# Performance work log

Measured on AMD Instinct MI355X. Metric: run time of the kernel, lower is better.

## Reference

```python
import jax, jax.numpy as jnp
import numpy as np

IN_CH = 32
OUT_CH = 32
M1, M2 = 32, 32
BS, H, W = 8, 256, 256


def setup_inputs() -> dict:
    key = jax.random.key(0)
    kx, kk = jax.random.split(key)
    x = jax.random.normal(kx, (BS, IN_CH, H, W), dtype=jnp.float32)
    # reset_parameters: randn * (1/(in_ch*out_ch)) + 1
    scale = 1.0 / (IN_CH * OUT_CH)
    kernel = jax.random.normal(kk, (2, 1, OUT_CH, M1, M2, 2), dtype=jnp.float32) * scale + 1.0
    r = jnp.float32(1.0)
    return {"x": x, "kernel": kernel, "r": r}


def reference(x, kernel, r):
    # view_as_complex: last dim of 2 -> complex, shape [2, 1, C, M1, M2]
    kc = (kernel[..., 0] + 1j * kernel[..., 1]).astype(jnp.complex64)
    # elementwise complex power kernel**r
    kc = jnp.power(kc, r)

    # forward 2D real FFT over spatial dims (ortho norm)
    x_ft = jnp.fft.rfftn(x, axes=(-2, -1), norm="ortho")  # [bs, C, H, W//2+1]
    Hf, Wr = x_ft.shape[-2], x_ft.shape[-1]
    n1 = min(Hf // 2, M1)
    n2 = min(Wr, M2)

    def mix(block, k):
        # fft over channel dim (-3), multiply by complex kernel, ifft back
        b = jnp.fft.fft(block, axis=-3, norm="ortho")
        b = b * k[..., :n1, :n2]
        return jnp.fft.ifft(b, axis=-3, norm="ortho")

    pos = mix(x_ft[..., :n1, :n2], kc[0])          # low positive freqs
    neg = mix(x_ft[..., Hf - n1:, :n2], kc[1])     # low negative freqs

    out_ft = jnp.zeros((x.shape[0], OUT_CH, Hf, Wr), dtype=jnp.complex64)
    out_ft = out_ft.at[..., :n1, :n2].set(pos)
    out_ft = out_ft.at[..., Hf - n1:, :n2].set(neg)

    # inverse real FFT back to spatial domain
    return jnp.fft.irfftn(out_ft, s=(x.shape[-2], x.shape[-1]), axes=(-2, -1), norm="ortho")
```

## Files before the change

### kernel.cpp

```cpp
#include <hip/hip_runtime.h>
#include <math.h>


#define TWO_PI 6.28318530717958647692f

typedef _Float16 half8 __attribute__((ext_vector_type(8)));
typedef float float4v __attribute__((ext_vector_type(4)));

__global__ __launch_bounds__(256) void kPX(const float* __restrict__ kin,
                                           const float* __restrict__ rp,
                                           float2* __restrict__ kp,
                                           _Float16* __restrict__ Bf) {
  const int tid = threadIdx.x;
  if (blockIdx.x < 256) {
    const int i = blockIdx.x * 256 + tid;
    const float r = rp[0];
    const float kr = kin[2 * i], ki = kin[2 * i + 1];
    const float m2 = fmaf(kr, kr, ki * ki);
    float2 o = make_float2(0.f, 0.f);
    if (m2 > 0.f) {
      const float lm = 0.5f * logf(m2);
      const float ang = atan2f(ki, kr);
      const float mag = expf(r * lm);
      float s, c;
      sincosf(r * ang, &s, &c);
      o = make_float2(mag * c, mag * s);
    }
    kp[i] = o;
  } else {
    const int f0 = ((blockIdx.x - 256) * 256 + tid) * 2;
#pragma unroll
    for (int u = 0; u < 2; ++u) {
      const int f = f0 + u;
      const int i = f & 7;
      const int lane = (f >> 3) & 63;
      const int kk = (f >> 9) & 1;
      const int n = f >> 10;
      const int k = kk * 32 + ((lane >> 4) << 3) + i;
      const int w = k >> 1, cs = k & 1;
      const int xc = n * 16 + (lane & 15);
      const float sc = (w ? 2.0f : 1.0f) / 256.0f;
      float s, c;
      sincosf(TWO_PI * (float)((w * xc) & 255) / 256.0f, &s, &c);
      Bf[f] = (_Float16)(cs ? (-s * sc) : (c * sc));
    }
  }
}

__global__ __launch_bounds__(256) void kA(const float* __restrict__ x,
                                          float2* __restrict__ z1) {
  __shared__ float xs[8192];
  const int tid = threadIdx.x;
  const long row0 = (long)blockIdx.x * 32;
  const float* xg = x + row0 * 256;
  {
    const int xl = tid & 31, rq = tid >> 5;
    const float* xgr = xg + rq * 4 * 256 + xl;
#pragma unroll
    for (int cb = 0; cb < 8; ++cb) {
      const int xc = xl + 32 * cb;
      const float4 v = make_float4(xgr[32 * cb], xgr[32 * cb + 256],
                                   xgr[32 * cb + 512], xgr[32 * cb + 768]);
      *(float4*)(xs + xc * 32 + 4 * ((rq + xc) & 7)) = v;
    }
  }
  __syncthreads();
  const float RT = 0.70710678118654752440f;
#pragma unroll
  for (int k = 0; k < 4; ++k) {
    const int i = tid + (k << 8);
    const int x1 = i >> 5, r = i & 31;
    float* base = xs + x1 * 32 + ((r + 4 * x1) & 31);
    const float a0 = base[0],        a1 = base[1024],     a2 = base[2048];
    const float a3 = base[3 * 1024], a4 = base[4 * 1024], a5 = base[5 * 1024];
    const float a6 = base[6 * 1024], a7 = base[7 * 1024];
    const float t0 = a0 + a4, t1 = a0 - a4, t2 = a2 + a6, t3 = a2 - a6;
    const float u0 = a1 + a5, u1 = a1 - a5, u2 = a3 + a7, u3 = a3 - a7;
    const float E0 = t0 + t2, O0 = u0 + u2;
    const float d1 = RT * (u1 - u3), d2 = RT * (u1 + u3);
    base[0]        = E0 + O0;
    base[1024]     = E0 - O0;
    base[2 * 1024] = t1 + d1;
    base[3 * 1024] = -(t3 + d2);
    base[4 * 1024] = t0 - t2;
    base[5 * 1024] = -(u0 - u2);
    base[6 * 1024] = t1 - d1;
    base[7 * 1024] = t3 - d2;
  }
  __syncthreads();
  const int w = tid & 31;
  const int r0 = (tid >> 5) << 2;
  const int p = w & 7;
  int pr, pi;
  float si;
  if (p == 0)      { pr = 0;           pi = 0;      si = 0.f; }
  else if (p == 4) { pr = 1;           pi = 1;      si = 0.f; }
  else if (p < 4)  { pr = 2 * p;       pi = pr + 1; si = 1.f; }
  else             { pr = 2 * (8 - p); pi = pr + 1; si = -1.f; }
  const char* ur = (const char*)xs + pr * 4096;
  const char* ui = (const char*)xs + pi * 4096;
  const char* urp[8];
  const char* uip[8];
#pragma unroll
  for (int j = 0; j < 8; ++j) {
    const int off = 4 * ((r0 + 4 * j) & 31) + 128 * j;
    urp[j] = ur + off;
    uip[j] = ui + off;
  }
  float s1, c1;
  sincosf(-TWO_PI * (float)w / 256.0f, &s1, &c1);
  float pc = 1.f, ps = 0.f;
  float Cr0 = 0, Cr1 = 0, Cr2 = 0, Cr3 = 0;
  float Ci0 = 0, Ci1 = 0, Ci2 = 0, Ci3 = 0;
#pragma unroll
  for (int bq = 0; bq < 4; ++bq) {
#pragma unroll
    for (int j = 0; j < 8; ++j) {
      const float4 Fr = *(const float4*)(urp[j] + bq * 1024);
      const float4 Fi = *(const float4*)(uip[j] + bq * 1024);
      const float qs = si * ps, qc = si * pc;
      Cr0 = fmaf(Fr.x, pc, fmaf(-Fi.x, qs, Cr0));
      Ci0 = fmaf(Fr.x, ps, fmaf( Fi.x, qc, Ci0));
      Cr1 = fmaf(Fr.y, pc, fmaf(-Fi.y, qs, Cr1));
      Ci1 = fmaf(Fr.y, ps, fmaf( Fi.y, qc, Ci1));
      Cr2 = fmaf(Fr.z, pc, fmaf(-Fi.z, qs, Cr2));
      Ci2 = fmaf(Fr.z, ps, fmaf( Fi.z, qc, Ci2));
      Cr3 = fmaf(Fr.w, pc, fmaf(-Fi.w, qs, Cr3));
      Ci3 = fmaf(Fr.w, ps, fmaf( Fi.w, qc, Ci3));
      const float tn = fmaf(pc, c1, -ps * s1);
      ps = fmaf(pc, s1, ps * c1);
      pc = tn;
    }
  }
  float2* o = z1 + (row0 + r0) * 32 + w;
  o[0]  = make_float2(Cr0, Ci0);
  o[32] = make_float2(Cr1, Ci1);
  o[64] = make_float2(Cr2, Ci2);
  o[96] = make_float2(Cr3, Ci3);
}

__global__ __launch_bounds__(256) void kB(const float2* __restrict__ z1,
                                          float2* __restrict__ z2) {
  __shared__ float2 zs[8192];
  const int tid = threadIdx.x;
  const int bc = blockIdx.x >> 1, th = blockIdx.x & 1;
  {
    const float4* s4 = (const float4*)(z1 + (long)bc * 8192);
    float4* d4 = (float4*)zs;
    for (int i = tid; i < 4096; i += 256) d4[i] = s4[i];
  }
  __syncthreads();
  const float RT = 0.70710678118654752440f;
#pragma unroll
  for (int e = 0; e < 4; ++e) {
    float2* base = zs + tid + (e << 8);
    float2 a[8];
#pragma unroll
    for (int j = 0; j < 8; ++j) a[j] = base[j * 1024];
    float2 t0 = make_float2(a[0].x + a[4].x, a[0].y + a[4].y);
    float2 t1 = make_float2(a[0].x - a[4].x, a[0].y - a[4].y);
    float2 t2 = make_float2(a[2].x + a[6].x, a[2].y + a[6].y);
    float2 t3 = make_float2(a[2].x - a[6].x, a[2].y - a[6].y);
    const float2 E0 = make_float2(t0.x + t2.x, t0.y + t2.y);
    const float2 E2 = make_float2(t0.x - t2.x, t0.y - t2.y);
    const float2 E1 = make_float2(t1.x + t3.y, t1.y - t3.x);
    const float2 E3 = make_float2(t1.x - t3.y, t1.y + t3.x);
    t0 = make_float2(a[1].x + a[5].x, a[1].y + a[5].y);
    t1 = make_float2(a[1].x - a[5].x, a[1].y - a[5].y);
    t2 = make_float2(a[3].x + a[7].x, a[3].y + a[7].y);
    t3 = make_float2(a[3].x - a[7].x, a[3].y - a[7].y);
    const float2 O0 = make_float2(t0.x + t2.x, t0.y + t2.y);
    const float2 O2 = make_float2(t0.x - t2.x, t0.y - t2.y);
    const float2 O1 = make_float2(t1.x + t3.y, t1.y - t3.x);
    const float2 O3 = make_float2(t1.x - t3.y, t1.y + t3.x);
    const float2 B0 = O0;
    const float2 B1 = make_float2(RT * (O1.x + O1.y), RT * (O1.y - O1.x));
    const float2 B2 = make_float2(O2.y, -O2.x);
    const float2 B3 = make_float2(RT * (O3.y - O3.x), -RT * (O3.x + O3.y));
    base[0]        = make_float2(E0.x + B0.x, E0.y + B0.y);
    base[1 * 1024] = make_float2(E1.x + B1.x, E1.y + B1.y);
    base[2 * 1024] = make_float2(E2.x + B2.x, E2.y + B2.y);
    base[3 * 1024] = make_float2(E3.x + B3.x, E3.y + B3.y);
    base[4 * 1024] = make_float2(E0.x - B0.x, E0.y - B0.y);
    base[5 * 1024] = make_float2(E1.x - B1.x, E1.y - B1.y);
    base[6 * 1024] = make_float2(E2.x - B2.x, E2.y - B2.y);
    base[7 * 1024] = make_float2(E3.x - B3.x, E3.y - B3.y);
  }
  __syncthreads();
  const int w = tid & 31;
  const int lt = tid >> 5;
  const int t0i = th * 32 + lt;
  const int hbase = th ? (192 + t0i) : t0i;
  float stc[4], sts[4], pcq[4], psq[4], ar[4], ai[4];
#pragma unroll
  for (int q = 0; q < 4; ++q) {
    sincosf(-TWO_PI * (float)(hbase + 8 * q) / 256.0f, &sts[q], &stc[q]);
    pcq[q] = 1.f; psq[q] = 0.f; ar[q] = 0.f; ai[q] = 0.f;
  }
  const float2* sp = zs + lt * 1024 + w;
  for (int y1 = 0; y1 < 32; ++y1) {
    const float2 v = sp[y1 * 32];
#pragma unroll
    for (int q = 0; q < 4; ++q) {
      ar[q] = fmaf(v.x, pcq[q], fmaf(-v.y, psq[q], ar[q]));
      ai[q] = fmaf(v.x, psq[q], fmaf( v.y, pcq[q], ai[q]));
      const float tn = fmaf(pcq[q], stc[q], -psq[q] * sts[q]);
      psq[q] = fmaf(pcq[q], sts[q], psq[q] * stc[q]);
      pcq[q] = tn;
    }
  }
  float2* dst = z2 + (long)bc * 2048 + t0i * 32 + w;
#pragma unroll
  for (int q = 0; q < 4; ++q) dst[q * 256] = make_float2(ar[q], ai[q]);
}

__global__ __launch_bounds__(256) void kC(const float2* __restrict__ z2,
                                          const float2* __restrict__ kp,
                                          float2* __restrict__ g) {
  __shared__ float2 z2s[8 * 33];
  __shared__ float2 fk[8 * 33];
  __shared__ float2 tw[32];
  const int tid = threadIdx.x;
  if (tid < 32) {
    float s, c;
    sincosf(-TWO_PI * (float)tid / 32.0f, &s, &c);
    tw[tid] = make_float2(c, s);
  }
  const int m0 = blockIdx.x * 8;
  const int b = m0 >> 11;
  const int twi = m0 & 2047;
  const int t = twi >> 5;
  const int w0 = twi & 31;
  const int s_ = t >> 5, tm = t & 31;
  {
    const int ci = tid >> 3, wj = tid & 7;
    z2s[wj * 33 + ci] = z2[((long)(b * 32 + ci)) * 2048 + t * 32 + w0 + wj];
  }
  __syncthreads();
  const int m = tid & 7;
  {
    const int cf = tid >> 3;
    float fr = 0, fi = 0;
    int i0 = 0;
#pragma unroll 8
    for (int ci = 0; ci < 32; ++ci) {
      const float2 z = z2s[m * 33 + ci];
      const float2 t0 = tw[i0]; i0 = (i0 + cf) & 31;
      fr = fmaf(z.x, t0.x, fmaf(-z.y, t0.y, fr));
      fi = fmaf(z.x, t0.y, fmaf( z.y, t0.x, fi));
    }
    const float2 k0 = kp[((s_ * 32 + cf) * 32 + tm) * 32 + w0 + m];
    fk[m * 33 + cf] = make_float2(fr * k0.x - fi * k0.y, fr * k0.y + fi * k0.x);
  }
  __syncthreads();
  {
    const int co = tid >> 3;
    float gr = 0, gi = 0;
    int i0 = 0;
#pragma unroll 8
    for (int cf = 0; cf < 32; ++cf) {
      const float2 f = fk[m * 33 + cf];
      const float2 t0 = tw[i0]; i0 = (i0 + co) & 31;
      gr = fmaf(f.x, t0.x, fmaf( f.y, t0.y, gr));
      gi = fmaf(f.y, t0.x, fmaf(-f.x, t0.y, gi));
    }
    const float SC = 1.0f / 8192.0f;
    g[((long)(b * 32 + co)) * 2048 + t * 32 + w0 + m] = make_float2(gr * SC, gi * SC);
  }
}

__global__ __launch_bounds__(512) void kDE2(const float2* __restrict__ g,
                                            const _Float16* __restrict__ Bf,
                                            float* __restrict__ out) {
  __shared__ float smem[32 * 260];
  __shared__ _Float16 tst2[32 * 68];
  float2* gs = (float2*)smem;
  float* ot = smem;
  const int tid = threadIdx.x;
  const int bc = blockIdx.x >> 1, yh = blockIdx.x & 1;
  const int lane = tid & 63, l15 = lane & 15, lg = lane >> 4;
  uint4 bfr[2][2];
#pragma unroll
  for (int nn = 0; nn < 2; ++nn)
#pragma unroll
    for (int kk = 0; kk < 2; ++kk) {
      const int n = 2 * (tid >> 6) + nn;
      bfr[nn][kk] = *(const uint4*)(Bf + (((n * 2 + kk) * 64) + lane) * 8);
    }
  {
    const float4* s4 = (const float4*)(g + (long)bc * 2048);
    float4* d4 = (float4*)gs;
    for (int i = tid; i < 1024; i += 512) d4[i] = s4[i];
  }
  __syncthreads();
  const int w = tid & 31;
  float Ur[2][8], Ui[2][8];
#pragma unroll
  for (int e = 0; e < 2; ++e) {
    const int y1 = (tid + (e << 9)) >> 5;
#pragma unroll
    for (int p = 0; p < 8; ++p) { Ur[e][p] = 0.f; Ui[e][p] = 0.f; }
    float s1, c1;
    sincosf(TWO_PI * (float)y1 / 256.0f, &s1, &c1);
    float pc = 1.f, ps = 0.f;
#pragma unroll
    for (int t = 0; t < 64; ++t) {
      if (t == 32) {
        float s2, c2;
        sincosf(TWO_PI * (float)((224 * y1) & 255) / 256.0f, &s2, &c2);
        pc = c2; ps = s2;
      }
      const float2 v = gs[t * 32 + w];
      const int k = t & 7;
      Ur[e][k] = fmaf(v.x, pc, fmaf(-v.y, ps, Ur[e][k]));
      Ui[e][k] = fmaf(v.x, ps, fmaf( v.y, pc, Ui[e][k]));
      const float tn = fmaf(pc, c1, -ps * s1);
      ps = fmaf(pc, s1, ps * c1);
      pc = tn;
    }
  }
  const long rb0 = (long)bc * 256;
#pragma unroll
  for (int yql = 0; yql < 4; ++yql) {
    const int yq = yh * 4 + yql;
    {
      float sqv, cqv;
      sincosf(TWO_PI * (float)yq / 8.0f, &sqv, &cqv);
#pragma unroll
      for (int e = 0; e < 2; ++e) {
        const int y1 = (tid + (e << 9)) >> 5;
        float tr = 0.f, ti = 0.f, qc = 1.f, qs = 0.f;
#pragma unroll
        for (int p = 0; p < 8; ++p) {
          tr = fmaf(Ur[e][p], qc, fmaf(-Ui[e][p], qs, tr));
          ti = fmaf(Ur[e][p], qs, fmaf( Ui[e][p], qc, ti));
          const float tn = fmaf(qc, cqv, -qs * sqv);
          qs = fmaf(qc, sqv, qs * cqv);
          qc = tn;
        }
        union { unsigned int u; _Float16 h[2]; } hu;
        hu.h[0] = (_Float16)tr;
        hu.h[1] = (_Float16)ti;
        *(unsigned int*)&tst2[y1 * 68 + 2 * w] = hu.u;
      }
    }
    __syncthreads();
    {
      half8 afr[2][2];
#pragma unroll
      for (int rt = 0; rt < 2; ++rt)
#pragma unroll
        for (int kk = 0; kk < 2; ++kk) {
          const _Float16* ap = tst2 + (rt * 16 + l15) * 68 + kk * 32 + lg * 8;
          const uint2 lo = *(const uint2*)ap;
          const uint2 hi = *(const uint2*)(ap + 4);
          uint4 u4;
          u4.x = lo.x; u4.y = lo.y; u4.z = hi.x; u4.w = hi.y;
          afr[rt][kk] = __builtin_bit_cast(half8, u4);
        }
#pragma unroll
      for (int rt = 0; rt < 2; ++rt)
#pragma unroll
        for (int nn = 0; nn < 2; ++nn) {
          float4v acc = {0.f, 0.f, 0.f, 0.f};
          acc = __builtin_amdgcn_mfma_f32_16x16x32_f16(
              afr[rt][0], __builtin_bit_cast(half8, bfr[nn][0]), acc, 0, 0, 0);
          acc = __builtin_amdgcn_mfma_f32_16x16x32_f16(
              afr[rt][1], __builtin_bit_cast(half8, bfr[nn][1]), acc, 0, 0, 0);
          const int n = 2 * (tid >> 6) + nn;
          const int col = n * 16 + l15;
          const int r0l = rt * 16 + lg * 4;
          ot[(r0l + 0) * 260 + col] = acc[0];
          ot[(r0l + 1) * 260 + col] = acc[1];
          ot[(r0l + 2) * 260 + col] = acc[2];
          ot[(r0l + 3) * 260 + col] = acc[3];
        }
    }
    __syncthreads();
    {
      const long rbase = rb0 + yq * 32;
#pragma unroll
      for (int rd = 0; rd < 4; ++rd) {
        const int f = tid + (rd << 9);
        const int row = f >> 6;
        const int c4 = f & 63;
        const float4 v = *(const float4*)(ot + row * 260 + c4 * 4);
        *(float4*)(out + (rbase + row) * 256 + c4 * 4) = v;
      }
    }
  }
}

extern "C" void kernel_launch(void* const* d_in, const int* in_sizes, int n_in,
                              void* d_out, int out_size, void* d_ws, size_t ws_size,
                              hipStream_t stream) {
  const float* x = (const float*)d_in[0];
  const float* kin = (const float*)d_in[1];
  const float* rp = (const float*)d_in[2];
  float* out = (float*)d_out;
  char* ws = (char*)d_ws;

  float2* z1 = (float2*)(ws);
  float2* z2 = (float2*)(ws + (16ull << 20));
  float2* kp = (float2*)(ws + (24ull << 20));
  _Float16* Bf = (_Float16*)(ws + (25ull << 20));
  float2* g  = (float2*)(ws);

  kPX<<<288, 256, 0, stream>>>(kin, rp, kp, Bf);
  kA<<<2048, 256, 0, stream>>>(x, z1);
  kB<<<512, 256, 0, stream>>>(z1, z2);
  kC<<<2048, 256, 0, stream>>>(z2, kp, g);
  kDE2<<<512, 512, 0, stream>>>(g, Bf, out);
}
```

Before: 182.8 us.

## Replace row-wise partial DFT in kA with fp16 MFMA matmul against twiddle table

```diff
diff --git a/kernel.cpp b/kernel.cpp
--- a/kernel.cpp
+++ b/kernel.cpp
@@ -10,7 +10,8 @@
 __global__ __launch_bounds__(256) void kPX(const float* __restrict__ kin,
                                            const float* __restrict__ rp,
                                            float2* __restrict__ kp,
-                                           _Float16* __restrict__ Bf) {
+                                           _Float16* __restrict__ Bf,
+                                           _Float16* __restrict__ Ef) {
   const int tid = threadIdx.x;
   if (blockIdx.x < 256) {
     const int i = blockIdx.x * 256 + tid;
@@ -27,7 +28,7 @@
       o = make_float2(mag * c, mag * s);
     }
     kp[i] = o;
-  } else {
+  } else if (blockIdx.x < 288) {
     const int f0 = ((blockIdx.x - 256) * 256 + tid) * 2;
 #pragma unroll
     for (int u = 0; u < 2; ++u) {
@@ -44,99 +45,69 @@
       sincosf(TWO_PI * (float)((w * xc) & 255) / 256.0f, &s, &c);
       Bf[f] = (_Float16)(cs ? (-s * sc) : (c * sc));
     }
-  }
-}
-
-__global__ __launch_bounds__(256) void kA(const float* __restrict__ x,
-                                          float2* __restrict__ z1) {
-  __shared__ float xs[8192];
+  } else {
+    const int f0 = ((blockIdx.x - 288) * 256 + tid) * 2;
+#pragma unroll
+    for (int u = 0; u < 2; ++u) {
+      const int f = f0 + u;
+      const int i = f & 7;
+      const int lane = (f >> 3) & 63;
+      const int seg = f >> 9;
+      const int kk = seg & 7, nn = seg >> 3;
+      const int k = kk * 32 + ((lane >> 4) << 3) + i;
+      const int n = nn * 16 + (lane & 15);
+      const int w = n >> 1, cs = n & 1;
+      float s, c;
+      sincosf(TWO_PI * (float)((w * k) & 255) / 256.0f, &s, &c);
+      Ef[f] = (_Float16)(cs ? -s : c);
+    }
+  }
+}
+
+__global__ __launch_bounds__(256) void kA3(const float* __restrict__ x,
+                                           const _Float16* __restrict__ Ef,
+                                           float* __restrict__ z1f) {
+  __shared__ _Float16 As[8192];
   const int tid = threadIdx.x;
   const long row0 = (long)blockIdx.x * 32;
-  const float* xg = x + row0 * 256;
-  {
-    const int xl = tid & 31, rq = tid >> 5;
-    const float* xgr = xg + rq * 4 * 256 + xl;
-#pragma unroll
-    for (int cb = 0; cb < 8; ++cb) {
-      const int xc = xl + 32 * cb;
-      const float4 v = make_float4(xgr[32 * cb], xgr[32 * cb + 256],
-                                   xgr[32 * cb + 512], xgr[32 * cb + 768]);
-      *(float4*)(xs + xc * 32 + 4 * ((rq + xc) & 7)) = v;
-    }
-  }
-  __syncthreads();
-  const float RT = 0.70710678118654752440f;
-#pragma unroll
-  for (int k = 0; k < 4; ++k) {
-    const int i = tid + (k << 8);
-    const int x1 = i >> 5, r = i & 31;
-    float* base = xs + x1 * 32 + ((r + 4 * x1) & 31);
-    const float a0 = base[0],        a1 = base[1024],     a2 = base[2048];
-    const float a3 = base[3 * 1024], a4 = base[4 * 1024], a5 = base[5 * 1024];
-    const float a6 = base[6 * 1024], a7 = base[7 * 1024];
-    const float t0 = a0 + a4, t1 = a0 - a4, t2 = a2 + a6, t3 = a2 - a6;
-    const float u0 = a1 + a5, u1 = a1 - a5, u2 = a3 + a7, u3 = a3 - a7;
-    const float E0 = t0 + t2, O0 = u0 + u2;
-    const float d1 = RT * (u1 - u3), d2 = RT * (u1 + u3);
-    base[0]        = E0 + O0;
-    base[1024]     = E0 - O0;
-    base[2 * 1024] = t1 + d1;
-    base[3 * 1024] = -(t3 + d2);
-    base[4 * 1024] = t0 - t2;
-    base[5 * 1024] = -(u0 - u2);
-    base[6 * 1024] = t1 - d1;
-    base[7 * 1024] = t3 - d2;
-  }
-  __syncthreads();
-  const int w = tid & 31;
-  const int r0 = (tid >> 5) << 2;
-  const int p = w & 7;
-  int pr, pi;
-  float si;
-  if (p == 0)      { pr = 0;           pi = 0;      si = 0.f; }
-  else if (p == 4) { pr = 1;           pi = 1;      si = 0.f; }
-  else if (p < 4)  { pr = 2 * p;       pi = pr + 1; si = 1.f; }
-  else             { pr = 2 * (8 - p); pi = pr + 1; si = -1.f; }
-  const char* ur = (const char*)xs + pr * 4096;
-  const char* ui = (const char*)xs + pi * 4096;
-  const char* urp[8];
-  const char* uip[8];
-#pragma unroll
-  for (int j = 0; j < 8; ++j) {
-    const int off = 4 * ((r0 + 4 * j) & 31) + 128 * j;
-    urp[j] = ur + off;
-    uip[j] = ui + off;
-  }
-  float s1, c1;
-  sincosf(-TWO_PI * (float)w / 256.0f, &s1, &c1);
-  float pc = 1.f, ps = 0.f;
-  float Cr0 = 0, Cr1 = 0, Cr2 = 0, Cr3 = 0;
-  float Ci0 = 0, Ci1 = 0, Ci2 = 0, Ci3 = 0;
-#pragma unroll
-  for (int bq = 0; bq < 4; ++bq) {
-#pragma unroll
-    for (int j = 0; j < 8; ++j) {
-      const float4 Fr = *(const float4*)(urp[j] + bq * 1024);
-      const float4 Fi = *(const float4*)(uip[j] + bq * 1024);
-      const float qs = si * ps, qc = si * pc;
-      Cr0 = fmaf(Fr.x, pc, fmaf(-Fi.x, qs, Cr0));
-      Ci0 = fmaf(Fr.x, ps, fmaf( Fi.x, qc, Ci0));
-      Cr1 = fmaf(Fr.y, pc, fmaf(-Fi.y, qs, Cr1));
-      Ci1 = fmaf(Fr.y, ps, fmaf( Fi.y, qc, Ci1));
-      Cr2 = fmaf(Fr.z, pc, fmaf(-Fi.z, qs, Cr2));
-      Ci2 = fmaf(Fr.z, ps, fmaf( Fi.z, qc, Ci2));
-      Cr3 = fmaf(Fr.w, pc, fmaf(-Fi.w, qs, Cr3));
-      Ci3 = fmaf(Fr.w, ps, fmaf( Fi.w, qc, Ci3));
-      const float tn = fmaf(pc, c1, -ps * s1);
-      ps = fmaf(pc, s1, ps * c1);
-      pc = tn;
-    }
-  }
-  float2* o = z1 + (row0 + r0) * 32 + w;
-  o[0]  = make_float2(Cr0, Ci0);
-  o[32] = make_float2(Cr1, Ci1);
-  o[64] = make_float2(Cr2, Ci2);
-  o[96] = make_float2(Cr3, Ci3);
+  const int lane = tid & 63, l15 = lane & 15, lg = lane >> 4;
+  const int nn = tid >> 6;
+  uint4 bfr[8];
+#pragma unroll
+  for (int kk = 0; kk < 8; ++kk)
+    bfr[kk] = *(const uint4*)(Ef + (((nn * 8 + kk) * 64) + lane) * 8);
+#pragma unroll
+  for (int q = 0; q < 4; ++q) {
+    const int fr = q * 256 + tid;
+    const int rt = fr >> 9, kk = (fr >> 6) & 7;
+    const int lgs = (fr >> 4) & 3, rl = fr & 15;
+    const float* xp = x + (row0 + rt * 16 + rl) * 256 + kk * 32 + lgs * 8;
+    const float4 v0 = *(const float4*)xp;
+    const float4 v1 = *(const float4*)(xp + 4);
+    union { uint4 u; _Float16 h[8]; } cv;
+    cv.h[0] = (_Float16)v0.x; cv.h[1] = (_Float16)v0.y;
+    cv.h[2] = (_Float16)v0.z; cv.h[3] = (_Float16)v0.w;
+    cv.h[4] = (_Float16)v1.x; cv.h[5] = (_Float16)v1.y;
+    cv.h[6] = (_Float16)v1.z; cv.h[7] = (_Float16)v1.w;
+    *(uint4*)(As + fr * 8) = cv.u;
+  }
+  __syncthreads();
+#pragma unroll
+  for (int rt = 0; rt < 2; ++rt) {
+    float4v acc = {0.f, 0.f, 0.f, 0.f};
+#pragma unroll
+    for (int kk = 0; kk < 8; ++kk) {
+      const half8 afr = *(const half8*)(As + ((rt * 8 + kk) * 64 + lane) * 8);
+      acc = __builtin_amdgcn_mfma_f32_16x16x32_f16(
+          afr, __builtin_bit_cast(half8, bfr[kk]), acc, 0, 0, 0);
+    }
+    const int n = nn * 16 + l15;
+    float* o = z1f + (row0 + rt * 16 + lg * 4) * 64 + n;
+    o[0]       = acc[0];
+    o[64]      = acc[1];
+    o[2 * 64]  = acc[2];
+    o[3 * 64]  = acc[3];
+  }
 }
 
 __global__ __launch_bounds__(256) void kB(const float2* __restrict__ z1,
@@ -404,10 +375,11 @@
   float2* z2 = (float2*)(ws + (16ull << 20));
   float2* kp = (float2*)(ws + (24ull << 20));
   _Float16* Bf = (_Float16*)(ws + (25ull << 20));
+  _Float16* Ef = (_Float16*)(ws + (26ull << 20));
   float2* g  = (float2*)(ws);
 
-  kPX<<<288, 256, 0, stream>>>(kin, rp, kp, Bf);
-  kA<<<2048, 256, 0, stream>>>(x, z1);
+  kPX<<<320, 256, 0, stream>>>(kin, rp, kp, Bf, Ef);
+  kA3<<<2048, 256, 0, stream>>>(x, Ef, (float*)z1);
   kB<<<512, 256, 0, stream>>>(z1, z2);
   kC<<<2048, 256, 0, stream>>>(z2, kp, g);
   kDE2<<<512, 512, 0, stream>>>(g, Bf, out);
```

Measured after the change: 177.5 us. 1.03x faster.
